# Kernel optimization log

Measured on AMD Instinct MI355X. Metric: run time of the kernel, lower is better.

The kernel has to match this reference:

```python
import jax, jax.numpy as jnp
import numpy as np

POS_IOU = 0.5
NEG_IOU = 0.4
REG_LOSS_WEIGHT = 1.0
B, N, C, T = 8, 65536, 80, 32
MIN_POS = 16


def _make_boxes(key, prefix, scale=640.0):
    k1, k2 = jax.random.split(key)
    cxcy = jax.random.uniform(k1, prefix + (2,), dtype=jnp.float32) * scale
    wh = jax.random.uniform(k2, prefix + (2,), minval=0.02, maxval=0.3, dtype=jnp.float32) * scale
    return jnp.concatenate([cxcy - 0.5 * wh, cxcy + 0.5 * wh], axis=-1)


def setup_inputs() -> dict:
    key = jax.random.key(0)
    ks = jax.random.split(key, 5)
    cls_output = jax.random.normal(ks[0], (B, N, C), jnp.float32)
    reg_output = jax.random.normal(ks[1], (B, N, 4), jnp.float32) * 0.1
    anchors = _make_boxes(ks[2], (N,))
    target_boxes = _make_boxes(ks[3], (B, T))
    target_labels = jax.random.randint(ks[4], (B, T), 1, C)  # labels >= 1 (non-empty images)
    return {"cls_output": cls_output, "reg_output": reg_output, "anchors": anchors,
            "target_boxes": target_boxes, "target_labels": target_labels}


def _decode_boxes(reg, anchors):
    # standard SSD decode; exact inverse of the encoding used for reg_targets
    aw = anchors[:, 2] - anchors[:, 0]
    ah = anchors[:, 3] - anchors[:, 1]
    acx = anchors[:, 0] + 0.5 * aw
    acy = anchors[:, 1] + 0.5 * ah
    cx = reg[:, 0] * aw + acx
    cy = reg[:, 1] * ah + acy
    w = jnp.exp(reg[:, 2]) * aw
    h = jnp.exp(reg[:, 3]) * ah
    return jnp.stack([cx - 0.5 * w, cy - 0.5 * h, cx + 0.5 * w, cy + 0.5 * h], axis=-1)


def _iou(a, b):
    # a: [N,4], b: [T,4] -> [N,T]
    lt = jnp.maximum(a[:, None, :2], b[None, :, :2])
    rb = jnp.minimum(a[:, None, 2:], b[None, :, 2:])
    wh = jnp.clip(rb - lt, 0.0)
    inter = wh[..., 0] * wh[..., 1]
    area_a = (a[:, 2] - a[:, 0]) * (a[:, 3] - a[:, 1])
    area_b = (b[:, 2] - b[:, 0]) * (b[:, 3] - b[:, 1])
    return inter / (area_a[:, None] + area_b[None, :] - inter + 1e-6)


def _focal_from_ce(ce, is_pos, alpha, gamma):
    p_t = jnp.exp(-ce)
    alpha_t = jnp.where(is_pos, alpha, 1.0 - alpha)
    return alpha_t * (1.0 - p_t) ** gamma * ce


def _per_image(cls_i, reg_i, boxes, labels, anchors):
    n = cls_i.shape[0]
    decoded = _decode_boxes(reg_i, anchors)
    ious = _iou(decoded, boxes)                       # [N,T]
    max_ious = ious.max(axis=1)
    max_idx = ious.argmax(axis=1)

    # positive selection with top-16 fallback
    pos_thr = max_ious >= POS_IOU
    _, top_idx = jax.lax.top_k(max_ious, MIN_POS)
    top_mask = jnp.zeros(n, bool).at[top_idx].set(True)
    pos_mask = jnp.where(pos_thr.sum() < MIN_POS, top_mask, pos_thr)
    num_pos = pos_mask.sum()

    # hard-negative mining: top (4*num_pos) non-positive anchors by IoU
    neg_scores = jnp.where(pos_mask, -jnp.inf, max_ious)
    order = jnp.argsort(-neg_scores)
    rank = jnp.zeros(n, jnp.int32).at[order].set(jnp.arange(n, dtype=jnp.int32))
    k = jnp.minimum(n - num_pos, 4 * num_pos)
    neg_mask = rank < k

    # focal classification loss (shared log_softmax)
    logp = jax.nn.log_softmax(cls_i, axis=-1)         # [N,C]
    anchor_labels = labels[max_idx]                   # [N]
    ce_pos = -jnp.take_along_axis(logp, anchor_labels[:, None], axis=1)[:, 0]
    ce_neg = -logp[:, 0]
    fl_pos = _focal_from_ce(ce_pos, anchor_labels > 0, 0.25, 2.0)
    fl_neg = _focal_from_ce(ce_neg, False, 0.1, 3.0)
    cls_pos = jnp.where(pos_mask, fl_pos, 0.0).sum()
    cls_neg = jnp.where(neg_mask, fl_neg, 0.0).sum()
    total_samples = jnp.maximum(num_pos + neg_mask.sum(), 1)
    cls_loss = (cls_pos + cls_neg) / total_samples

    gt = boxes[max_idx]                               # [N,4]
    aw = anchors[:, 2] - anchors[:, 0]
    ah = anchors[:, 3] - anchors[:, 1]
    acx = anchors[:, 0] + 0.5 * aw
    acy = anchors[:, 1] + 0.5 * ah
    gw = gt[:, 2] - gt[:, 0]
    gh = gt[:, 3] - gt[:, 1]
    gcx = gt[:, 0] + 0.5 * gw
    gcy = gt[:, 1] + 0.5 * gh
    reg_t = jnp.stack([(gcx - acx) / (aw + 1e-6),
                       (gcy - acy) / (ah + 1e-6),
                       jnp.log(gw / (aw + 1e-6)),
                       jnp.log(gh / (ah + 1e-6))], axis=-1)
    diff = jnp.abs(reg_i - reg_t)
    sl1 = jnp.where(diff < 1.0, 0.5 * diff * diff, diff - 0.5)
    reg_loss = jnp.where(pos_mask[:, None], sl1, 0.0).sum() / (num_pos + 1e-6)
    return cls_loss, reg_loss, num_pos


def reference(cls_output, reg_output, anchors, target_boxes, target_labels):
    cls_l, reg_l, npos = jax.vmap(_per_image, in_axes=(0, 0, 0, 0, None))(
        cls_output, reg_output, target_boxes, target_labels, anchors)
    total_pos = npos.sum()
    cls_final = cls_l.mean()
    reg_final = jnp.where(total_pos > 0, reg_l.mean(), 0.0)
    bsz = cls_output.shape[0]
    reg_weight = jnp.minimum(1.0, total_pos.astype(jnp.float32) / (100.0 * bsz))
    total_loss = cls_final + reg_weight * REG_LOSS_WEIGHT * reg_final
    return total_loss, cls_final, reg_final, total_pos
```

## Files before the change

kernel.cpp:

```cpp
#include <hip/hip_runtime.h>
#include <math.h>

#define BB 8
#define NN 65536
#define CC 80
#define TT 32
#define MINPOS 16
#define TIECAP 4096

__global__ __launch_bounds__(256) void k_prep(
    const float* __restrict__ reg, const float* __restrict__ anchors,
    const float* __restrict__ tboxes, const int* __restrict__ tlabels,
    float* __restrict__ miou_out, float* __restrict__ sl1_out,
    unsigned char* __restrict__ lbl_out,
    unsigned* __restrict__ gHist, int* __restrict__ posCnt)
{
    const int b   = blockIdx.y;
    const int tid = threadIdx.x;
    const int a   = blockIdx.x * 256 + tid;

    __shared__ float4 tb[TT];
    __shared__ float  tarea[TT];
    __shared__ int    tl[TT];
    __shared__ unsigned lh[512];
    __shared__ int    s_pc;

    if (tid < TT) {
        float4 t = ((const float4*)(tboxes + (size_t)b * TT * 4))[tid];
        tb[tid] = t;
        tarea[tid] = (t.z - t.x) * (t.w - t.y);
        tl[tid] = tlabels[b * TT + tid];
    }
    lh[tid] = 0u; lh[tid + 256] = 0u;
    if (tid == 0) s_pc = 0;
    __syncthreads();

    float4 r  = ((const float4*)reg)[(size_t)b * NN + a];
    float4 an = ((const float4*)anchors)[a];
    float aw = an.z - an.x, ah = an.w - an.y;
    float acx = an.x + 0.5f * aw, acy = an.y + 0.5f * ah;
    float cx = r.x * aw + acx, cy = r.y * ah + acy;
    float w = expf(r.z) * aw, hh = expf(r.w) * ah;
    float dx0 = cx - 0.5f * w, dy0 = cy - 0.5f * hh;
    float dx1 = cx + 0.5f * w, dy1 = cy + 0.5f * hh;
    float areaA = (dx1 - dx0) * (dy1 - dy0);

    float mi = -1.0f; int mix = 0;
    #pragma unroll 8
    for (int t = 0; t < TT; ++t) {
        float4 bx = tb[t];
        float ltx = fmaxf(dx0, bx.x), lty = fmaxf(dy0, bx.y);
        float rbx = fminf(dx1, bx.z), rby = fminf(dy1, bx.w);
        float iw = fmaxf(rbx - ltx, 0.0f), ih = fmaxf(rby - lty, 0.0f);
        float inter = iw * ih;
        float iou = inter / (areaA + tarea[t] - inter + 1e-6f);
        if (iou > mi) { mi = iou; mix = t; }
    }

    float4 gt = tb[mix];
    float gw = gt.z - gt.x, gh = gt.w - gt.y;
    float gcx = gt.x + 0.5f * gw, gcy = gt.y + 0.5f * gh;
    float t0 = (gcx - acx) / (aw + 1e-6f);
    float t1 = (gcy - acy) / (ah + 1e-6f);
    float t2 = logf(gw / (aw + 1e-6f));
    float t3 = logf(gh / (ah + 1e-6f));
    float d0 = fabsf(r.x - t0), d1 = fabsf(r.y - t1);
    float d2 = fabsf(r.z - t2), d3 = fabsf(r.w - t3);
    float sl1v = (d0 < 1.0f ? 0.5f * d0 * d0 : d0 - 0.5f)
               + (d1 < 1.0f ? 0.5f * d1 * d1 : d1 - 0.5f)
               + (d2 < 1.0f ? 0.5f * d2 * d2 : d2 - 0.5f)
               + (d3 < 1.0f ? 0.5f * d3 * d3 : d3 - 0.5f);

    miou_out[(size_t)b * NN + a] = mi;
    sl1_out[(size_t)b * NN + a]  = sl1v;
    lbl_out[(size_t)b * NN + a]  = (unsigned char)tl[mix];

    atomicAdd(&lh[__float_as_uint(mi) >> 21], 1u);
    unsigned long long bal = __ballot(mi >= 0.5f);
    if ((tid & 63) == 0) atomicAdd(&s_pc, __popcll(bal));
    __syncthreads();

    if (lh[tid])       atomicAdd(&gHist[b * 512 + tid],       lh[tid]);
    if (lh[tid + 256]) atomicAdd(&gHist[b * 512 + tid + 256], lh[tid + 256]);
    if (tid == 0) atomicAdd(&posCnt[b], s_pc);
}

__device__ __forceinline__ void scan_hist64(unsigned* hist, int NB, int tid, int* sh_s)
{
    if (tid < 64) {
        const int cs = NB / 64;
        const int base = tid * cs;
        int csum = 0;
        for (int j = 0; j < cs; ++j) csum += (int)hist[base + j];
        int sfx = csum;
        #pragma unroll
        for (int off = 1; off < 64; off <<= 1) {
            int o = __shfl_down(sfx, off);
            if (tid + off < 64) sfx += o;
        }
        const int excl = sfx - csum;
        const int need = sh_s[2];
        int acc = excl;
        for (int j = cs - 1; j >= 0; --j) {
            int hcnt = (int)hist[base + j];
            int S = acc + hcnt;
            if (acc < need && S >= need) { sh_s[0] = base + j; sh_s[1] = acc; }
            acc = S;
        }
    }
}

__device__ __forceinline__ void radix_select(
    const float* __restrict__ vals, const unsigned char* __restrict__ mask,
    int mode, int kk, int tid,
    unsigned* hist, int* sh_s, unsigned* sh_u)
{
    if (tid == 0) { sh_u[0] = 0u; sh_u[1] = 0u; sh_s[2] = kk; }
    __syncthreads();
    #pragma unroll
    for (int rnd = 0; rnd < 3; ++rnd) {
        const int sh = (rnd == 0) ? 21 : ((rnd == 1) ? 10 : 0);
        const int NB = (rnd == 2) ? 1024 : 2048;
        hist[tid] = 0u; hist[tid + 1024] = 0u;
        __syncthreads();
        const unsigned pref = sh_u[0], pmask = sh_u[1];
        for (int i = tid; i < NN; i += 1024) {
            bool c = (mode == 0) ? true
                   : (mode == 1) ? (vals[i] < 0.5f)
                                 : (mask[i] != (unsigned char)1);
            if (c) {
                unsigned u = __float_as_uint(vals[i]);
                if ((u & pmask) == pref)
                    atomicAdd(&hist[(u >> sh) & (unsigned)(NB - 1)], 1u);
            }
        }
        __syncthreads();
        scan_hist64(hist, NB, tid, sh_s);
        __syncthreads();
        if (tid == 0) {
            sh_u[0] |= ((unsigned)sh_s[0]) << sh;
            sh_u[1] |= ((unsigned)(NB - 1)) << sh;
            sh_s[2] -= sh_s[1];
        }
        __syncthreads();
    }
}

__global__ __launch_bounds__(1024) void k_select(
    const float* __restrict__ miou_all, const float* __restrict__ sl1_all,
    const unsigned char* __restrict__ lbl_all,
    const unsigned* __restrict__ gHist, const int* __restrict__ posCnt,
    unsigned char* __restrict__ mask_all,
    unsigned* __restrict__ list_all, int* __restrict__ listCnt,
    int* __restrict__ numpos, int* __restrict__ knum, float* __restrict__ accum)
{
    const int b = blockIdx.x;
    const int tid = threadIdx.x;
    const float* miou = miou_all + (size_t)b * NN;
    const float* sl1  = sl1_all  + (size_t)b * NN;
    const unsigned char* lbl = lbl_all + (size_t)b * NN;
    unsigned char* mask = mask_all + (size_t)b * NN;
    unsigned* list = list_all + (size_t)b * NN;

    __shared__ unsigned hist[2048];
    __shared__ int sh_s[3];
    __shared__ unsigned sh_u[2];
    __shared__ int wtot[16];
    __shared__ int sh_ties;
    __shared__ unsigned tieU[TIECAP];
    __shared__ int tieI[TIECAP];
    __shared__ int sh_tc;
    __shared__ int sh_lc;
    __shared__ float wred[16];

    const int pc = posCnt[b];
    const bool fallback = (pc < MINPOS);
    float accR = 0.0f;
    int np, kk;

    if (tid == 0) sh_lc = 0;

    if (!fallback) {
        np = pc;
        kk = NN - np; if (4 * np < kk) kk = 4 * np;

        if (tid < 512) {
            unsigned v = gHist[b * 512 + tid];
            hist[tid] = (tid <= 503) ? v : 0u;
        }
        if (tid == 0) { sh_s[2] = kk; sh_tc = 0; }
        __syncthreads();
        scan_hist64(hist, 512, tid, sh_s);
        __syncthreads();
        const unsigned pivotBin = (unsigned)sh_s[0];
        if (tid == 0) sh_s[2] -= sh_s[1];
        hist[tid] = 0u; hist[tid + 1024] = 0u;
        __syncthreads();

        for (int i = tid; i < NN; i += 1024) {
            unsigned u = __float_as_uint(miou[i]);
            if ((u >> 21) == pivotBin) atomicAdd(&hist[(u >> 10) & 2047u], 1u);
        }
        __syncthreads();
        scan_hist64(hist, 2048, tid, sh_s);
        __syncthreads();
        const unsigned pivot22 = (pivotBin << 11) | (unsigned)sh_s[0];
        const int rem = sh_s[2] - sh_s[1];

        for (int i = tid; i < NN; i += 1024) {
            float v = miou[i];
            unsigned u = __float_as_uint(v);
            if (v >= 0.5f) {
                accR += sl1[i];
                int t = atomicAdd(&sh_lc, 1);
                list[t] = (unsigned)i | 0x10000u | ((unsigned)lbl[i] << 17);
            } else {
                unsigned p = u >> 10;
                if (p > pivot22) {
                    int t = atomicAdd(&sh_lc, 1);
                    list[t] = (unsigned)i;
                } else if (p == pivot22) {
                    int t = atomicAdd(&sh_tc, 1);
                    if (t < TIECAP) { tieU[t] = u; tieI[t] = i; }
                }
            }
        }
        __syncthreads();
        int tc = sh_tc; if (tc > TIECAP) tc = TIECAP;
        for (int t = tid; t < tc; t += 1024) {
            unsigned ut = tieU[t]; int it = tieI[t];
            int rank = 0;
            for (int j = 0; j < tc; ++j) {
                unsigned uj = tieU[j]; int ij = tieI[j];
                rank += (uj > ut || (uj == ut && ij < it)) ? 1 : 0;
            }
            if (rank < rem) {
                int t2 = atomicAdd(&sh_lc, 1);
                list[t2] = (unsigned)it;
            }
        }
    } else {
        radix_select(miou, mask, 0, MINPOS, tid, hist, sh_s, sh_u);
        {
            const unsigned vb = sh_u[0];
            const int rem = sh_s[2];
            if (tid == 0) sh_ties = 0;
            __syncthreads();
            for (int base = 0; base < NN; base += 1024) {
                const int i = base + tid;
                const unsigned u = __float_as_uint(miou[i]);
                const bool tie = (u == vb);
                unsigned long long bal = __ballot(tie);
                const int wave = tid >> 6, lane = tid & 63;
                if (lane == 0) wtot[wave] = __popcll(bal);
                __syncthreads();
                int wexcl = 0;
                for (int wv = 0; wv < wave; ++wv) wexcl += wtot[wv];
                const int myexcl = sh_ties + wexcl + __popcll(bal & ((1ull << lane) - 1ull));
                const bool sel = (u > vb) || (tie && myexcl < rem);
                mask[i] = sel ? (unsigned char)1 : (unsigned char)0;
                __syncthreads();
                if (tid == 0) { int ts = 0; for (int wv = 0; wv < 16; ++wv) ts += wtot[wv]; sh_ties += ts; }
                __syncthreads();
            }
        }
        np = MINPOS;
        kk = NN - np; if (4 * np < kk) kk = 4 * np;
        radix_select(miou, mask, 2, kk, tid, hist, sh_s, sh_u);
        {
            const unsigned vb = sh_u[0];
            const int rem = sh_s[2];
            if (tid == 0) sh_ties = 0;
            __syncthreads();
            for (int base = 0; base < NN; base += 1024) {
                const int i = base + tid;
                const unsigned u = __float_as_uint(miou[i]);
                const bool pos = (mask[i] == (unsigned char)1);
                const bool cand = !pos;
                const bool tie = cand && (u == vb);
                unsigned long long bal = __ballot(tie);
                const int wave = tid >> 6, lane = tid & 63;
                if (lane == 0) wtot[wave] = __popcll(bal);
                __syncthreads();
                int wexcl = 0;
                for (int wv = 0; wv < wave; ++wv) wexcl += wtot[wv];
                const int myexcl = sh_ties + wexcl + __popcll(bal & ((1ull << lane) - 1ull));
                const bool neg = cand && ((u > vb) || (tie && myexcl < rem));
                mask[i] = pos ? (unsigned char)1 : (neg ? (unsigned char)2 : (unsigned char)0);
                __syncthreads();
                if (tid == 0) { int ts = 0; for (int wv = 0; wv < 16; ++wv) ts += wtot[wv]; sh_ties += ts; }
                __syncthreads();
            }
        }
        __syncthreads();
        for (int i = tid; i < NN; i += 1024) {
            unsigned char m = mask[i];
            if (m == (unsigned char)1) {
                accR += sl1[i];
                int t = atomicAdd(&sh_lc, 1);
                list[t] = (unsigned)i | 0x10000u | ((unsigned)lbl[i] << 17);
            } else if (m == (unsigned char)2) {
                int t = atomicAdd(&sh_lc, 1);
                list[t] = (unsigned)i;
            }
        }
    }

    #pragma unroll
    for (int off = 32; off > 0; off >>= 1) accR += __shfl_down(accR, off);
    const int lane = tid & 63, wave = tid >> 6;
    if (lane == 0) wred[wave] = accR;
    __syncthreads();
    if (tid == 0) {
        float sR = 0.0f;
        for (int w = 0; w < 16; ++w) sR += wred[w];
        accum[b * 3 + 0] = 0.0f;
        accum[b * 3 + 1] = 0.0f;
        accum[b * 3 + 2] = sR;
        numpos[b] = np;
        knum[b] = kk;
        listCnt[b] = sh_lc;
    }
}

__global__ __launch_bounds__(256) void k_cls2(
    const float* __restrict__ cls, const unsigned* __restrict__ list_all,
    const int* __restrict__ listCnt, float* __restrict__ accum)
{
    const int b   = blockIdx.y;
    const int n   = listCnt[b];
    const int al  = threadIdx.x >> 2;
    const int sub = threadIdx.x & 3;
    const unsigned* list = list_all + (size_t)b * NN;

    float aP = 0.0f, aN = 0.0f;
    for (int e = blockIdx.x * 64 + al; e < n; e += gridDim.x * 64) {
        unsigned ent = list[e];
        int a = (int)(ent & 0xFFFFu);
        size_t row = (size_t)b * NN + a;
        const float4* rowp = (const float4*)(cls + row * CC);
        float4 v0 = rowp[sub];
        float4 v1 = rowp[sub + 4];
        float4 v2 = rowp[sub + 8];
        float4 v3 = rowp[sub + 12];
        float4 v4 = rowp[sub + 16];
        float mx = fmaxf(fmaxf(fmaxf(v0.x, v0.y), fmaxf(v0.z, v0.w)),
                   fmaxf(fmaxf(fmaxf(v1.x, v1.y), fmaxf(v1.z, v1.w)),
                   fmaxf(fmaxf(fmaxf(v2.x, v2.y), fmaxf(v2.z, v2.w)),
                   fmaxf(fmaxf(fmaxf(v3.x, v3.y), fmaxf(v3.z, v3.w)),
                         fmaxf(fmaxf(v4.x, v4.y), fmaxf(v4.z, v4.w))))));
        float sm = expf(v0.x - mx) + expf(v0.y - mx) + expf(v0.z - mx) + expf(v0.w - mx)
                 + expf(v1.x - mx) + expf(v1.y - mx) + expf(v1.z - mx) + expf(v1.w - mx)
                 + expf(v2.x - mx) + expf(v2.y - mx) + expf(v2.z - mx) + expf(v2.w - mx)
                 + expf(v3.x - mx) + expf(v3.y - mx) + expf(v3.z - mx) + expf(v3.w - mx)
                 + expf(v4.x - mx) + expf(v4.y - mx) + expf(v4.z - mx) + expf(v4.w - mx);
        #pragma unroll
        for (int off = 1; off < 4; off <<= 1) {
            float m2 = __shfl_xor(mx, off);
            float s2 = __shfl_xor(sm, off);
            float nm = fmaxf(mx, m2);
            sm = sm * expf(mx - nm) + s2 * expf(m2 - nm);
            mx = nm;
        }
        if (sub == 0) {
            float lse = mx + logf(sm);
            if (ent & 0x10000u) {
                int lab = (int)((ent >> 17) & 0x7Fu);
                float ce = lse - cls[row * CC + lab];
                float pt = expf(-ce);
                float o  = 1.0f - pt;
                aP += (lab > 0 ? 0.25f : 0.75f) * o * o * ce;
            } else {
                float ce = lse - v0.x;
                float pt = expf(-ce);
                float o  = 1.0f - pt;
                aN += 0.9f * o * o * o * ce;
            }
        }
    }

    #pragma unroll
    for (int off = 32; off > 0; off >>= 1) {
        aP += __shfl_down(aP, off);
        aN += __shfl_down(aN, off);
    }
    __shared__ float wp[4], wn[4];
    const int lane = threadIdx.x & 63, wave = threadIdx.x >> 6;
    if (lane == 0) { wp[wave] = aP; wn[wave] = aN; }
    __syncthreads();
    if (threadIdx.x == 0) {
        atomicAdd(&accum[b * 3 + 0], wp[0] + wp[1] + wp[2] + wp[3]);
        atomicAdd(&accum[b * 3 + 1], wn[0] + wn[1] + wn[2] + wn[3]);
    }
}

__global__ void k_finalize(const float* __restrict__ accum,
                           const int* __restrict__ numpos,
                           const int* __restrict__ knum,
                           float* __restrict__ out)
{
    if (threadIdx.x == 0 && blockIdx.x == 0) {
        float clsf = 0.0f, regf = 0.0f;
        int tp = 0;
        for (int b = 0; b < BB; ++b) {
            float cp = accum[b * 3 + 0];
            float cn = accum[b * 3 + 1];
            float rs = accum[b * 3 + 2];
            int np = numpos[b], kk = knum[b];
            int ts = np + kk; if (ts < 1) ts = 1;
            clsf += (cp + cn) / (float)ts;
            regf += rs / ((float)np + 1e-6f);
            tp += np;
        }
        clsf *= (1.0f / BB);
        regf *= (1.0f / BB);
        float reg_final = (tp > 0) ? regf : 0.0f;
        float rw = fminf(1.0f, (float)tp / (100.0f * BB));
        out[0] = clsf + rw * reg_final;
        out[1] = clsf;
        out[2] = reg_final;
        out[3] = (float)tp;
    }
}

extern "C" void kernel_launch(void* const* d_in, const int* in_sizes, int n_in,
                              void* d_out, int out_size, void* d_ws, size_t ws_size,
                              hipStream_t stream)
{
    const float* cls     = (const float*)d_in[0];
    const float* reg     = (const float*)d_in[1];
    const float* anchors = (const float*)d_in[2];
    const float* tboxes  = (const float*)d_in[3];
    const int*   tlabels = (const int*)d_in[4];

    const size_t PL = (size_t)BB * NN * 4;
    char* ws = (char*)d_ws;
    float* sl1  = (float*)(ws);
    float* miou = (float*)(ws + PL);
    unsigned* list = (unsigned*)(ws + 2 * PL);
    unsigned char* lbl  = (unsigned char*)(ws + 3 * PL);
    unsigned char* mask = (unsigned char*)(ws + 3 * PL + PL / 4);
    char* tail = ws + 3 * PL + PL / 2;
    unsigned* gHist = (unsigned*)tail;
    int*   posCnt  = (int*)(tail + 16384);
    int*   listCnt = (int*)(tail + 16384 + 64);
    int*   numpos  = (int*)(tail + 16384 + 128);
    int*   knum    = (int*)(tail + 16384 + 192);
    float* accum   = (float*)(tail + 16384 + 256);
    float* out     = (float*)d_out;

    hipMemsetAsync(gHist, 0, 16384 + 64, stream);

    k_prep<<<dim3(NN / 256, BB), 256, 0, stream>>>(reg, anchors, tboxes, tlabels,
                                                   miou, sl1, lbl, gHist, posCnt);
    k_select<<<BB, 1024, 0, stream>>>(miou, sl1, lbl, gHist, posCnt, mask,
                                      list, listCnt, numpos, knum, accum);
    k_cls2<<<dim3(128, BB), 256, 0, stream>>>(cls, list, listCnt, accum);
    k_finalize<<<1, 64, 0, stream>>>(accum, numpos, knum, out);
}
```

Measured before the change: 327.5 us.

## Split per-image selection into multi-block fine-hist, compaction and tie-rank kernels

The single 8-block k_select kernel is replaced by grid-parallel kernels: a fine histogram pass, a compaction pass that also recomputes the argmax target, smooth-L1 and label only for positive anchors, and a small tie-ranking kernel. k_prep now writes only the max IoU per anchor and uses a hardware reciprocal, which drops the sl1 and label stores and the regression math for every anchor. This spreads the previously serial per-image scan over many CUs, at the cost of more kernel launches and recomputing IoU for positives. The approximate reciprocal may change IoU bits near thresholds and tie ordering.

```diff
diff --git a/kernel.cpp b/kernel.cpp
--- a/kernel.cpp
+++ b/kernel.cpp
@@ -8,28 +8,27 @@
 #define MINPOS 16
 #define TIECAP 4096
 
+__device__ __forceinline__ float frcp(float x) { return __builtin_amdgcn_rcpf(x); }
+
 __global__ __launch_bounds__(256) void k_prep(
     const float* __restrict__ reg, const float* __restrict__ anchors,
-    const float* __restrict__ tboxes, const int* __restrict__ tlabels,
-    float* __restrict__ miou_out, float* __restrict__ sl1_out,
-    unsigned char* __restrict__ lbl_out,
-    unsigned* __restrict__ gHist, int* __restrict__ posCnt)
+    const float* __restrict__ tboxes,
+    float* __restrict__ miou_out, unsigned* __restrict__ gHist,
+    int* __restrict__ posCnt)
 {
     const int b   = blockIdx.y;
     const int tid = threadIdx.x;
     const int a   = blockIdx.x * 256 + tid;
 
     __shared__ float4 tb[TT];
-    __shared__ float  tarea[TT];
-    __shared__ int    tl[TT];
+    __shared__ float  tareaE[TT];
     __shared__ unsigned lh[512];
     __shared__ int    s_pc;
 
     if (tid < TT) {
         float4 t = ((const float4*)(tboxes + (size_t)b * TT * 4))[tid];
         tb[tid] = t;
-        tarea[tid] = (t.z - t.x) * (t.w - t.y);
-        tl[tid] = tlabels[b * TT + tid];
+        tareaE[tid] = (t.z - t.x) * (t.w - t.y) + 1e-6f;
     }
     lh[tid] = 0u; lh[tid + 256] = 0u;
     if (tid == 0) s_pc = 0;
@@ -45,7 +44,7 @@
     float dx1 = cx + 0.5f * w, dy1 = cy + 0.5f * hh;
     float areaA = (dx1 - dx0) * (dy1 - dy0);
 
-    float mi = -1.0f; int mix = 0;
+    float mi = 0.0f;
     #pragma unroll 8
     for (int t = 0; t < TT; ++t) {
         float4 bx = tb[t];
@@ -53,28 +52,12 @@
         float rbx = fminf(dx1, bx.z), rby = fminf(dy1, bx.w);
         float iw = fmaxf(rbx - ltx, 0.0f), ih = fmaxf(rby - lty, 0.0f);
         float inter = iw * ih;
-        float iou = inter / (areaA + tarea[t] - inter + 1e-6f);
-        if (iou > mi) { mi = iou; mix = t; }
-    }
-
-    float4 gt = tb[mix];
-    float gw = gt.z - gt.x, gh = gt.w - gt.y;
-    float gcx = gt.x + 0.5f * gw, gcy = gt.y + 0.5f * gh;
-    float t0 = (gcx - acx) / (aw + 1e-6f);
-    float t1 = (gcy - acy) / (ah + 1e-6f);
-    float t2 = logf(gw / (aw + 1e-6f));
-    float t3 = logf(gh / (ah + 1e-6f));
-    float d0 = fabsf(r.x - t0), d1 = fabsf(r.y - t1);
-    float d2 = fabsf(r.z - t2), d3 = fabsf(r.w - t3);
-    float sl1v = (d0 < 1.0f ? 0.5f * d0 * d0 : d0 - 0.5f)
-               + (d1 < 1.0f ? 0.5f * d1 * d1 : d1 - 0.5f)
-               + (d2 < 1.0f ? 0.5f * d2 * d2 : d2 - 0.5f)
-               + (d3 < 1.0f ? 0.5f * d3 * d3 : d3 - 0.5f);
+        float den = areaA + tareaE[t] - inter;
+        float iou = inter * frcp(den);
+        mi = fmaxf(mi, iou);
+    }
 
     miou_out[(size_t)b * NN + a] = mi;
-    sl1_out[(size_t)b * NN + a]  = sl1v;
-    lbl_out[(size_t)b * NN + a]  = (unsigned char)tl[mix];
-
     atomicAdd(&lh[__float_as_uint(mi) >> 21], 1u);
     unsigned long long bal = __ballot(mi >= 0.5f);
     if ((tid & 63) == 0) atomicAdd(&s_pc, __popcll(bal));
@@ -110,6 +93,215 @@
     }
 }
 
+__global__ __launch_bounds__(256) void k_finehist(
+    const float* __restrict__ miou_all, const unsigned* __restrict__ gHist,
+    const int* __restrict__ posCnt, unsigned* __restrict__ fineHist)
+{
+    const int b = blockIdx.y;
+    const int tid = threadIdx.x;
+    const int pc = posCnt[b];
+    if (pc < MINPOS) return;
+    const int np = pc;
+    int kk = NN - np; if (4 * np < kk) kk = 4 * np;
+
+    __shared__ unsigned hist[512];
+    __shared__ int sh_s[3];
+    hist[tid]       = (tid <= 503)       ? gHist[b * 512 + tid]       : 0u;
+    hist[tid + 256] = (tid + 256 <= 503) ? gHist[b * 512 + tid + 256] : 0u;
+    if (tid == 0) sh_s[2] = kk;
+    __syncthreads();
+    scan_hist64(hist, 512, tid, sh_s);
+    __syncthreads();
+    const unsigned pivotBin = (unsigned)sh_s[0];
+
+    const float* miou = miou_all + (size_t)b * NN;
+    const int base = blockIdx.x * 2048;
+    for (int i = base + tid; i < base + 2048; i += 256) {
+        unsigned u = __float_as_uint(miou[i]);
+        if ((u >> 21) == pivotBin)
+            atomicAdd(&fineHist[b * 2048 + ((u >> 10) & 2047u)], 1u);
+    }
+}
+
+__global__ __launch_bounds__(256) void k_compact(
+    const float* __restrict__ reg, const float* __restrict__ anchors,
+    const float* __restrict__ tboxes, const int* __restrict__ tlabels,
+    const float* __restrict__ miou_all,
+    const unsigned* __restrict__ gHist, const unsigned* __restrict__ fineHist,
+    const int* __restrict__ posCnt,
+    unsigned* __restrict__ list_all, int* __restrict__ listCnt,
+    unsigned* __restrict__ tieU_all, int* __restrict__ tieI_all,
+    int* __restrict__ tieCnt,
+    int* __restrict__ numpos, int* __restrict__ knum, float* __restrict__ accum)
+{
+    const int b = blockIdx.y;
+    const int tid = threadIdx.x;
+    const int pc = posCnt[b];
+    if (pc < MINPOS) return;
+    const int np = pc;
+    int kk = NN - np; if (4 * np < kk) kk = 4 * np;
+
+    __shared__ float4 tb[TT];
+    __shared__ float  tareaE[TT];
+    __shared__ int    tl[TT];
+    __shared__ unsigned hist[2048];
+    __shared__ unsigned lbuf[2048];
+    __shared__ int sh_s[3];
+    __shared__ int sh_cnt, sh_base;
+    __shared__ float wred[4];
+
+    if (tid < TT) {
+        float4 t = ((const float4*)(tboxes + (size_t)b * TT * 4))[tid];
+        tb[tid] = t;
+        tareaE[tid] = (t.z - t.x) * (t.w - t.y) + 1e-6f;
+        tl[tid] = tlabels[b * TT + tid];
+    }
+    hist[tid]       = (tid <= 503)       ? gHist[b * 512 + tid]       : 0u;
+    hist[tid + 256] = (tid + 256 <= 503) ? gHist[b * 512 + tid + 256] : 0u;
+    if (tid == 0) { sh_s[2] = kk; sh_cnt = 0; }
+    __syncthreads();
+    scan_hist64(hist, 512, tid, sh_s);
+    __syncthreads();
+    const unsigned pivotBin = (unsigned)sh_s[0];
+    const int needB = kk - sh_s[1];
+    __syncthreads();
+    for (int k = tid; k < 2048; k += 256) hist[k] = fineHist[b * 2048 + k];
+    if (tid == 0) sh_s[2] = needB;
+    __syncthreads();
+    scan_hist64(hist, 2048, tid, sh_s);
+    __syncthreads();
+    const unsigned pivot22 = (pivotBin << 11) | (unsigned)sh_s[0];
+
+    float accR = 0.0f;
+    const float* miou = miou_all + (size_t)b * NN;
+    const int base = blockIdx.x * 2048;
+    for (int i = base + tid; i < base + 2048; i += 256) {
+        float v = miou[i];
+        unsigned u = __float_as_uint(v);
+        if (v >= 0.5f) {
+            float4 r  = ((const float4*)reg)[(size_t)b * NN + i];
+            float4 an = ((const float4*)anchors)[i];
+            float aw = an.z - an.x, ah = an.w - an.y;
+            float acx = an.x + 0.5f * aw, acy = an.y + 0.5f * ah;
+            float cx = r.x * aw + acx, cy = r.y * ah + acy;
+            float w = expf(r.z) * aw, hh2 = expf(r.w) * ah;
+            float dx0 = cx - 0.5f * w, dy0 = cy - 0.5f * hh2;
+            float dx1 = cx + 0.5f * w, dy1 = cy + 0.5f * hh2;
+            float areaA = (dx1 - dx0) * (dy1 - dy0);
+            float mi = 0.0f; int mix = 0;
+            #pragma unroll 8
+            for (int t = 0; t < TT; ++t) {
+                float4 bx = tb[t];
+                float ltx = fmaxf(dx0, bx.x), lty = fmaxf(dy0, bx.y);
+                float rbx = fminf(dx1, bx.z), rby = fminf(dy1, bx.w);
+                float iw = fmaxf(rbx - ltx, 0.0f), ih = fmaxf(rby - lty, 0.0f);
+                float inter = iw * ih;
+                float den = areaA + tareaE[t] - inter;
+                float iou = inter * frcp(den);
+                if (iou > mi) { mi = iou; mix = t; }
+            }
+            float4 gt = tb[mix];
+            float gw = gt.z - gt.x, gh = gt.w - gt.y;
+            float gcx = gt.x + 0.5f * gw, gcy = gt.y + 0.5f * gh;
+            float t0 = (gcx - acx) / (aw + 1e-6f);
+            float t1 = (gcy - acy) / (ah + 1e-6f);
+            float t2 = logf(gw / (aw + 1e-6f));
+            float t3 = logf(gh / (ah + 1e-6f));
+            float d0 = fabsf(r.x - t0), d1 = fabsf(r.y - t1);
+            float d2 = fabsf(r.z - t2), d3 = fabsf(r.w - t3);
+            accR += (d0 < 1.0f ? 0.5f * d0 * d0 : d0 - 0.5f)
+                  + (d1 < 1.0f ? 0.5f * d1 * d1 : d1 - 0.5f)
+                  + (d2 < 1.0f ? 0.5f * d2 * d2 : d2 - 0.5f)
+                  + (d3 < 1.0f ? 0.5f * d3 * d3 : d3 - 0.5f);
+            int t4 = atomicAdd(&sh_cnt, 1);
+            lbuf[t4] = (unsigned)i | 0x10000u | ((unsigned)tl[mix] << 17);
+        } else {
+            unsigned p = u >> 10;
+            if (p > pivot22) {
+                int t = atomicAdd(&sh_cnt, 1);
+                lbuf[t] = (unsigned)i;
+            } else if (p == pivot22) {
+                int t = atomicAdd(&tieCnt[b], 1);
+                if (t < TIECAP) {
+                    tieU_all[b * TIECAP + t] = u;
+                    tieI_all[b * TIECAP + t] = i;
+                }
+            }
+        }
+    }
+    __syncthreads();
+    const int cnt = sh_cnt;
+    if (tid == 0) sh_base = atomicAdd(&listCnt[b], cnt);
+    __syncthreads();
+    unsigned* list = list_all + (size_t)b * NN;
+    for (int k = tid; k < cnt; k += 256) list[sh_base + k] = lbuf[k];
+
+    #pragma unroll
+    for (int off = 32; off > 0; off >>= 1) accR += __shfl_down(accR, off);
+    const int lane = tid & 63, wave = tid >> 6;
+    if (lane == 0) wred[wave] = accR;
+    __syncthreads();
+    if (tid == 0) {
+        atomicAdd(&accum[b * 3 + 2], wred[0] + wred[1] + wred[2] + wred[3]);
+        if (blockIdx.x == 0) { numpos[b] = np; knum[b] = kk; }
+    }
+}
+
+__global__ __launch_bounds__(256) void k_tierank(
+    const unsigned* __restrict__ gHist, const unsigned* __restrict__ fineHist,
+    const int* __restrict__ posCnt,
+    const unsigned* __restrict__ tieU_all, const int* __restrict__ tieI_all,
+    const int* __restrict__ tieCnt,
+    unsigned* __restrict__ list_all, int* __restrict__ listCnt)
+{
+    const int b = blockIdx.x;
+    const int tid = threadIdx.x;
+    const int pc = posCnt[b];
+    if (pc < MINPOS) return;
+    const int np = pc;
+    int kk = NN - np; if (4 * np < kk) kk = 4 * np;
+
+    __shared__ unsigned hist[2048];
+    __shared__ int sh_s[3];
+    __shared__ unsigned tu[TIECAP];
+    __shared__ int ti[TIECAP];
+
+    hist[tid]       = (tid <= 503)       ? gHist[b * 512 + tid]       : 0u;
+    hist[tid + 256] = (tid + 256 <= 503) ? gHist[b * 512 + tid + 256] : 0u;
+    if (tid == 0) sh_s[2] = kk;
+    __syncthreads();
+    scan_hist64(hist, 512, tid, sh_s);
+    __syncthreads();
+    const int needB = kk - sh_s[1];
+    __syncthreads();
+    for (int k = tid; k < 2048; k += 256) hist[k] = fineHist[b * 2048 + k];
+    if (tid == 0) sh_s[2] = needB;
+    __syncthreads();
+    scan_hist64(hist, 2048, tid, sh_s);
+    __syncthreads();
+    const int rem = needB - sh_s[1];
+
+    int c = tieCnt[b]; if (c > TIECAP) c = TIECAP;
+    for (int k = tid; k < c; k += 256) {
+        tu[k] = tieU_all[b * TIECAP + k];
+        ti[k] = tieI_all[b * TIECAP + k];
+    }
+    __syncthreads();
+    unsigned* list = list_all + (size_t)b * NN;
+    for (int t = tid; t < c; t += 256) {
+        unsigned ut = tu[t]; int it = ti[t];
+        int rank = 0;
+        for (int j = 0; j < c; ++j) {
+            unsigned uj = tu[j]; int ij = ti[j];
+            rank += (uj > ut || (uj == ut && ij < it)) ? 1 : 0;
+        }
+        if (rank < rem) {
+            int p = atomicAdd(&listCnt[b], 1);
+            list[p] = (unsigned)it;
+        }
+    }
+}
+
 __device__ __forceinline__ void radix_select(
     const float* __restrict__ vals, const unsigned char* __restrict__ mask,
     int mode, int kk, int tid,
@@ -125,9 +317,7 @@
         __syncthreads();
         const unsigned pref = sh_u[0], pmask = sh_u[1];
         for (int i = tid; i < NN; i += 1024) {
-            bool c = (mode == 0) ? true
-                   : (mode == 1) ? (vals[i] < 0.5f)
-                                 : (mask[i] != (unsigned char)1);
+            bool c = (mode == 0) ? true : (mask[i] != (unsigned char)1);
             if (c) {
                 unsigned u = __float_as_uint(vals[i]);
                 if ((u & pmask) == pref)
@@ -146,163 +336,135 @@
     }
 }
 
-__global__ __launch_bounds__(1024) void k_select(
-    const float* __restrict__ miou_all, const float* __restrict__ sl1_all,
-    const unsigned char* __restrict__ lbl_all,
-    const unsigned* __restrict__ gHist, const int* __restrict__ posCnt,
-    unsigned char* __restrict__ mask_all,
+__global__ __launch_bounds__(1024) void k_fallback(
+    const float* __restrict__ reg, const float* __restrict__ anchors,
+    const float* __restrict__ tboxes, const int* __restrict__ tlabels,
+    const float* __restrict__ miou_all, unsigned char* __restrict__ mask_all,
+    const int* __restrict__ posCnt,
     unsigned* __restrict__ list_all, int* __restrict__ listCnt,
     int* __restrict__ numpos, int* __restrict__ knum, float* __restrict__ accum)
 {
     const int b = blockIdx.x;
     const int tid = threadIdx.x;
+    if (posCnt[b] >= MINPOS) return;
+
     const float* miou = miou_all + (size_t)b * NN;
-    const float* sl1  = sl1_all  + (size_t)b * NN;
-    const unsigned char* lbl = lbl_all + (size_t)b * NN;
     unsigned char* mask = mask_all + (size_t)b * NN;
     unsigned* list = list_all + (size_t)b * NN;
 
+    __shared__ float4 tb[TT];
+    __shared__ float  tareaE[TT];
+    __shared__ int    tl[TT];
     __shared__ unsigned hist[2048];
     __shared__ int sh_s[3];
     __shared__ unsigned sh_u[2];
     __shared__ int wtot[16];
     __shared__ int sh_ties;
-    __shared__ unsigned tieU[TIECAP];
-    __shared__ int tieI[TIECAP];
-    __shared__ int sh_tc;
-    __shared__ int sh_lc;
     __shared__ float wred[16];
 
-    const int pc = posCnt[b];
-    const bool fallback = (pc < MINPOS);
+    if (tid < TT) {
+        float4 t = ((const float4*)(tboxes + (size_t)b * TT * 4))[tid];
+        tb[tid] = t;
+        tareaE[tid] = (t.z - t.x) * (t.w - t.y) + 1e-6f;
+        tl[tid] = tlabels[b * TT + tid];
+    }
+    __syncthreads();
+
+    radix_select(miou, mask, 0, MINPOS, tid, hist, sh_s, sh_u);
+    {
+        const unsigned vb = sh_u[0];
+        const int rem = sh_s[2];
+        if (tid == 0) sh_ties = 0;
+        __syncthreads();
+        for (int base = 0; base < NN; base += 1024) {
+            const int i = base + tid;
+            const unsigned u = __float_as_uint(miou[i]);
+            const bool tie = (u == vb);
+            unsigned long long bal = __ballot(tie);
+            const int wave = tid >> 6, lane = tid & 63;
+            if (lane == 0) wtot[wave] = __popcll(bal);
+            __syncthreads();
+            int wexcl = 0;
+            for (int wv = 0; wv < wave; ++wv) wexcl += wtot[wv];
+            const int myexcl = sh_ties + wexcl + __popcll(bal & ((1ull << lane) - 1ull));
+            const bool sel = (u > vb) || (tie && myexcl < rem);
+            mask[i] = sel ? (unsigned char)1 : (unsigned char)0;
+            __syncthreads();
+            if (tid == 0) { int ts = 0; for (int wv = 0; wv < 16; ++wv) ts += wtot[wv]; sh_ties += ts; }
+            __syncthreads();
+        }
+    }
+    const int np = MINPOS;
+    int kk = NN - np; if (4 * np < kk) kk = 4 * np;
+    radix_select(miou, mask, 2, kk, tid, hist, sh_s, sh_u);
+    {
+        const unsigned vb = sh_u[0];
+        const int rem = sh_s[2];
+        if (tid == 0) sh_ties = 0;
+        __syncthreads();
+        for (int base = 0; base < NN; base += 1024) {
+            const int i = base + tid;
+            const unsigned u = __float_as_uint(miou[i]);
+            const bool pos = (mask[i] == (unsigned char)1);
+            const bool cand = !pos;
+            const bool tie = cand && (u == vb);
+            unsigned long long bal = __ballot(tie);
+            const int wave = tid >> 6, lane = tid & 63;
+            if (lane == 0) wtot[wave] = __popcll(bal);
+            __syncthreads();
+            int wexcl = 0;
+            for (int wv = 0; wv < wave; ++wv) wexcl += wtot[wv];
+            const int myexcl = sh_ties + wexcl + __popcll(bal & ((1ull << lane) - 1ull));
+            const bool neg = cand && ((u > vb) || (tie && myexcl < rem));
+            mask[i] = pos ? (unsigned char)1 : (neg ? (unsigned char)2 : (unsigned char)0);
+            __syncthreads();
+            if (tid == 0) { int ts = 0; for (int wv = 0; wv < 16; ++wv) ts += wtot[wv]; sh_ties += ts; }
+            __syncthreads();
+        }
+    }
+
     float accR = 0.0f;
-    int np, kk;
-
-    if (tid == 0) sh_lc = 0;
-
-    if (!fallback) {
-        np = pc;
-        kk = NN - np; if (4 * np < kk) kk = 4 * np;
-
-        if (tid < 512) {
-            unsigned v = gHist[b * 512 + tid];
-            hist[tid] = (tid <= 503) ? v : 0u;
-        }
-        if (tid == 0) { sh_s[2] = kk; sh_tc = 0; }
-        __syncthreads();
-        scan_hist64(hist, 512, tid, sh_s);
-        __syncthreads();
-        const unsigned pivotBin = (unsigned)sh_s[0];
-        if (tid == 0) sh_s[2] -= sh_s[1];
-        hist[tid] = 0u; hist[tid + 1024] = 0u;
-        __syncthreads();
-
-        for (int i = tid; i < NN; i += 1024) {
-            unsigned u = __float_as_uint(miou[i]);
-            if ((u >> 21) == pivotBin) atomicAdd(&hist[(u >> 10) & 2047u], 1u);
-        }
-        __syncthreads();
-        scan_hist64(hist, 2048, tid, sh_s);
-        __syncthreads();
-        const unsigned pivot22 = (pivotBin << 11) | (unsigned)sh_s[0];
-        const int rem = sh_s[2] - sh_s[1];
-
-        for (int i = tid; i < NN; i += 1024) {
-            float v = miou[i];
-            unsigned u = __float_as_uint(v);
-            if (v >= 0.5f) {
-                accR += sl1[i];
-                int t = atomicAdd(&sh_lc, 1);
-                list[t] = (unsigned)i | 0x10000u | ((unsigned)lbl[i] << 17);
-            } else {
-                unsigned p = u >> 10;
-                if (p > pivot22) {
-                    int t = atomicAdd(&sh_lc, 1);
-                    list[t] = (unsigned)i;
-                } else if (p == pivot22) {
-                    int t = atomicAdd(&sh_tc, 1);
-                    if (t < TIECAP) { tieU[t] = u; tieI[t] = i; }
-                }
+    for (int i = tid; i < NN; i += 1024) {
+        unsigned char m = mask[i];
+        if (m == (unsigned char)1) {
+            float4 r  = ((const float4*)reg)[(size_t)b * NN + i];
+            float4 an = ((const float4*)anchors)[i];
+            float aw = an.z - an.x, ah = an.w - an.y;
+            float acx = an.x + 0.5f * aw, acy = an.y + 0.5f * ah;
+            float cx = r.x * aw + acx, cy = r.y * ah + acy;
+            float w = expf(r.z) * aw, hh2 = expf(r.w) * ah;
+            float dx0 = cx - 0.5f * w, dy0 = cy - 0.5f * hh2;
+            float dx1 = cx + 0.5f * w, dy1 = cy + 0.5f * hh2;
+            float areaA = (dx1 - dx0) * (dy1 - dy0);
+            float mi = 0.0f; int mix = 0;
+            for (int t = 0; t < TT; ++t) {
+                float4 bx = tb[t];
+                float ltx = fmaxf(dx0, bx.x), lty = fmaxf(dy0, bx.y);
+                float rbx = fminf(dx1, bx.z), rby = fminf(dy1, bx.w);
+                float iw = fmaxf(rbx - ltx, 0.0f), ih = fmaxf(rby - lty, 0.0f);
+                float inter = iw * ih;
+                float den = areaA + tareaE[t] - inter;
+                float iou = inter * frcp(den);
+                if (iou > mi) { mi = iou; mix = t; }
             }
-        }
-        __syncthreads();
-        int tc = sh_tc; if (tc > TIECAP) tc = TIECAP;
-        for (int t = tid; t < tc; t += 1024) {
-            unsigned ut = tieU[t]; int it = tieI[t];
-            int rank = 0;
-            for (int j = 0; j < tc; ++j) {
-                unsigned uj = tieU[j]; int ij = tieI[j];
-                rank += (uj > ut || (uj == ut && ij < it)) ? 1 : 0;
-            }
-            if (rank < rem) {
-                int t2 = atomicAdd(&sh_lc, 1);
-                list[t2] = (unsigned)it;
-            }
-        }
-    } else {
-        radix_select(miou, mask, 0, MINPOS, tid, hist, sh_s, sh_u);
-        {
-            const unsigned vb = sh_u[0];
-            const int rem = sh_s[2];
-            if (tid == 0) sh_ties = 0;
-            __syncthreads();
-            for (int base = 0; base < NN; base += 1024) {
-                const int i = base + tid;
-                const unsigned u = __float_as_uint(miou[i]);
-                const bool tie = (u == vb);
-                unsigned long long bal = __ballot(tie);
-                const int wave = tid >> 6, lane = tid & 63;
-                if (lane == 0) wtot[wave] = __popcll(bal);
-                __syncthreads();
-                int wexcl = 0;
-                for (int wv = 0; wv < wave; ++wv) wexcl += wtot[wv];
-                const int myexcl = sh_ties + wexcl + __popcll(bal & ((1ull << lane) - 1ull));
-                const bool sel = (u > vb) || (tie && myexcl < rem);
-                mask[i] = sel ? (unsigned char)1 : (unsigned char)0;
-                __syncthreads();
-                if (tid == 0) { int ts = 0; for (int wv = 0; wv < 16; ++wv) ts += wtot[wv]; sh_ties += ts; }
-                __syncthreads();
-            }
-        }
-        np = MINPOS;
-        kk = NN - np; if (4 * np < kk) kk = 4 * np;
-        radix_select(miou, mask, 2, kk, tid, hist, sh_s, sh_u);
-        {
-            const unsigned vb = sh_u[0];
-            const int rem = sh_s[2];
-            if (tid == 0) sh_ties = 0;
-            __syncthreads();
-            for (int base = 0; base < NN; base += 1024) {
-                const int i = base + tid;
-                const unsigned u = __float_as_uint(miou[i]);
-                const bool pos = (mask[i] == (unsigned char)1);
-                const bool cand = !pos;
-                const bool tie = cand && (u == vb);
-                unsigned long long bal = __ballot(tie);
-                const int wave = tid >> 6, lane = tid & 63;
-                if (lane == 0) wtot[wave] = __popcll(bal);
-                __syncthreads();
-                int wexcl = 0;
-                for (int wv = 0; wv < wave; ++wv) wexcl += wtot[wv];
-                const int myexcl = sh_ties + wexcl + __popcll(bal & ((1ull << lane) - 1ull));
-                const bool neg = cand && ((u > vb) || (tie && myexcl < rem));
-                mask[i] = pos ? (unsigned char)1 : (neg ? (unsigned char)2 : (unsigned char)0);
-                __syncthreads();
-                if (tid == 0) { int ts = 0; for (int wv = 0; wv < 16; ++wv) ts += wtot[wv]; sh_ties += ts; }
-                __syncthreads();
-            }
-        }
-        __syncthreads();
-        for (int i = tid; i < NN; i += 1024) {
-            unsigned char m = mask[i];
-            if (m == (unsigned char)1) {
-                accR += sl1[i];
-                int t = atomicAdd(&sh_lc, 1);
-                list[t] = (unsigned)i | 0x10000u | ((unsigned)lbl[i] << 17);
-            } else if (m == (unsigned char)2) {
-                int t = atomicAdd(&sh_lc, 1);
-                list[t] = (unsigned)i;
-            }
+            float4 gt = tb[mix];
+            float gw = gt.z - gt.x, gh = gt.w - gt.y;
+            float gcx = gt.x + 0.5f * gw, gcy = gt.y + 0.5f * gh;
+            float t0 = (gcx - acx) / (aw + 1e-6f);
+            float t1 = (gcy - acy) / (ah + 1e-6f);
+            float t2 = logf(gw / (aw + 1e-6f));
+            float t3 = logf(gh / (ah + 1e-6f));
+            float d0 = fabsf(r.x - t0), d1 = fabsf(r.y - t1);
+            float d2 = fabsf(r.z - t2), d3 = fabsf(r.w - t3);
+            accR += (d0 < 1.0f ? 0.5f * d0 * d0 : d0 - 0.5f)
+                  + (d1 < 1.0f ? 0.5f * d1 * d1 : d1 - 0.5f)
+                  + (d2 < 1.0f ? 0.5f * d2 * d2 : d2 - 0.5f)
+                  + (d3 < 1.0f ? 0.5f * d3 * d3 : d3 - 0.5f);
+            int t = atomicAdd(&listCnt[b], 1);
+            list[t] = (unsigned)i | 0x10000u | ((unsigned)tl[mix] << 17);
+        } else if (m == (unsigned char)2) {
+            int t = atomicAdd(&listCnt[b], 1);
+            list[t] = (unsigned)i;
         }
     }
 
@@ -314,12 +476,9 @@
     if (tid == 0) {
         float sR = 0.0f;
         for (int w = 0; w < 16; ++w) sR += wred[w];
-        accum[b * 3 + 0] = 0.0f;
-        accum[b * 3 + 1] = 0.0f;
         accum[b * 3 + 2] = sR;
         numpos[b] = np;
         knum[b] = kk;
-        listCnt[b] = sh_lc;
     }
 }
 
@@ -365,7 +524,7 @@
         if (sub == 0) {
             float lse = mx + logf(sm);
             if (ent & 0x10000u) {
-                int lab = (int)((ent >> 17) & 0x7Fu);
+                int lab = (int)((ent >> 17) & 0xFFu);
                 float ce = lse - cls[row * CC + lab];
                 float pt = expf(-ce);
                 float o  = 1.0f - pt;
@@ -435,26 +594,36 @@
 
     const size_t PL = (size_t)BB * NN * 4;
     char* ws = (char*)d_ws;
-    float* sl1  = (float*)(ws);
-    float* miou = (float*)(ws + PL);
-    unsigned* list = (unsigned*)(ws + 2 * PL);
-    unsigned char* lbl  = (unsigned char*)(ws + 3 * PL);
-    unsigned char* mask = (unsigned char*)(ws + 3 * PL + PL / 4);
-    char* tail = ws + 3 * PL + PL / 2;
-    unsigned* gHist = (unsigned*)tail;
-    int*   posCnt  = (int*)(tail + 16384);
-    int*   listCnt = (int*)(tail + 16384 + 64);
-    int*   numpos  = (int*)(tail + 16384 + 128);
-    int*   knum    = (int*)(tail + 16384 + 192);
-    float* accum   = (float*)(tail + 16384 + 256);
+    float*    miou = (float*)(ws);
+    unsigned* list = (unsigned*)(ws + PL);
+    unsigned char* mask = (unsigned char*)(ws + 2 * PL);
+    unsigned* tieU = (unsigned*)(ws + 2 * PL + PL / 4);
+    int*      tieI = (int*)(ws + 2 * PL + PL / 4 + (size_t)BB * TIECAP * 4);
+    char* Z = ws + 2 * PL + PL / 4 + 2 * (size_t)BB * TIECAP * 4;
+    unsigned* gHist    = (unsigned*)Z;
+    unsigned* fineHist = (unsigned*)(Z + 16384);
+    char* ctr = Z + 16384 + 65536;
+    int*   posCnt  = (int*)(ctr);
+    int*   listCnt = (int*)(ctr + 32);
+    int*   tieCnt  = (int*)(ctr + 64);
+    int*   numpos  = (int*)(ctr + 96);
+    int*   knum    = (int*)(ctr + 128);
+    float* accum   = (float*)(ctr + 160);
     float* out     = (float*)d_out;
 
-    hipMemsetAsync(gHist, 0, 16384 + 64, stream);
-
-    k_prep<<<dim3(NN / 256, BB), 256, 0, stream>>>(reg, anchors, tboxes, tlabels,
-                                                   miou, sl1, lbl, gHist, posCnt);
-    k_select<<<BB, 1024, 0, stream>>>(miou, sl1, lbl, gHist, posCnt, mask,
-                                      list, listCnt, numpos, knum, accum);
+    hipMemsetAsync(Z, 0, 16384 + 65536 + 256, stream);
+
+    k_prep<<<dim3(NN / 256, BB), 256, 0, stream>>>(reg, anchors, tboxes,
+                                                   miou, gHist, posCnt);
+    k_finehist<<<dim3(32, BB), 256, 0, stream>>>(miou, gHist, posCnt, fineHist);
+    k_compact<<<dim3(32, BB), 256, 0, stream>>>(reg, anchors, tboxes, tlabels,
+                                                miou, gHist, fineHist, posCnt,
+                                                list, listCnt, tieU, tieI, tieCnt,
+                                                numpos, knum, accum);
+    k_tierank<<<BB, 256, 0, stream>>>(gHist, fineHist, posCnt, tieU, tieI, tieCnt,
+                                      list, listCnt);
+    k_fallback<<<BB, 1024, 0, stream>>>(reg, anchors, tboxes, tlabels, miou, mask,
+                                        posCnt, list, listCnt, numpos, knum, accum);
     k_cls2<<<dim3(128, BB), 256, 0, stream>>>(cls, list, listCnt, accum);
     k_finalize<<<1, 64, 0, stream>>>(accum, numpos, knum, out);
 }
```

New measurement: 301.5 us. 7.9% less time.
